# Kernel tuning notes

Hardware: AMD Instinct MI355X
Metric: run time of the kernel (lower is better)

## Reference

```python
import jax, jax.numpy as jnp
import numpy as np

NUM_HEADS = 4
HEAD_DIM = 64
BN_EPS = 1e-5

def _leaky_relu(x, slope=0.2):
    return jnp.where(x >= 0, x, slope * x)

def _gat_conv(x, W, a_src, a_dst, src, dst):
    # x: [N, F_in], W: [F_out, F_in], a_*: [H, D]; edges src/dst: [E]
    N = x.shape[0]
    h = (x @ W.T).reshape(N, NUM_HEADS, HEAD_DIM)          # [N, H, D]
    s_src = jnp.einsum('nhd,hd->nh', h, a_src)              # [N, H]
    s_dst = jnp.einsum('nhd,hd->nh', h, a_dst)              # [N, H]
    e = _leaky_relu(s_src[src] + s_dst[dst])                # [E, H]
    # segment softmax over edges grouped by dst; torch index_reduce_ starts
    # from zeros (include_self=True) -> max with 0
    e_max = jnp.maximum(jax.ops.segment_max(e, dst, num_segments=N), 0.0)
    e_exp = jnp.exp(e - e_max[dst])                         # [E, H]
    e_sum = jax.ops.segment_sum(e_exp, dst, num_segments=N) # [N, H]
    alpha = e_exp / jnp.maximum(e_sum[dst], 1e-9)           # [E, H]
    msg = h[src] * alpha[..., None]                         # [E, H, D]
    out = jax.ops.segment_sum(msg, dst, num_segments=N)     # [N, H, D]
    return out.reshape(N, NUM_HEADS * HEAD_DIM)

def _bn_eval(x, gamma, beta, mean, var):
    return (x - mean) * jax.lax.rsqrt(var + BN_EPS) * gamma + beta

def _elu(x):
    return jnp.where(x > 0, x, jnp.expm1(x))

def setup_inputs() -> dict:
    key = jax.random.key(0)
    ks = jax.random.split(key, 12)
    N, E, IN, HID, OUT = 50000, 500000, 256, 256, 64
    s = 0.05
    return {
        'x': jax.random.normal(ks[0], (N, IN), jnp.float32),
        'edge_index': jax.random.randint(ks[1], (2, E), 0, N, jnp.int64),
        'W1': jax.random.normal(ks[2], (HID, IN), jnp.float32) * s,
        'a_src1': jax.random.normal(ks[3], (NUM_HEADS, HEAD_DIM), jnp.float32) * s,
        'a_dst1': jax.random.normal(ks[4], (NUM_HEADS, HEAD_DIM), jnp.float32) * s,
        'bn1_gamma': jnp.ones((HID,), jnp.float32),
        'bn1_beta': jnp.zeros((HID,), jnp.float32),
        'bn1_mean': jnp.zeros((HID,), jnp.float32),
        'bn1_var': jnp.ones((HID,), jnp.float32),
        'W2': jax.random.normal(ks[5], (HID, HID), jnp.float32) * s,
        'a_src2': jax.random.normal(ks[6], (NUM_HEADS, HEAD_DIM), jnp.float32) * s,
        'a_dst2': jax.random.normal(ks[7], (NUM_HEADS, HEAD_DIM), jnp.float32) * s,
        'bn2_gamma': jnp.ones((HID,), jnp.float32),
        'bn2_beta': jnp.zeros((HID,), jnp.float32),
        'bn2_mean': jnp.zeros((HID,), jnp.float32),
        'bn2_var': jnp.ones((HID,), jnp.float32),
        'Wc': jax.random.normal(ks[8], (OUT, HID), jnp.float32) * s,
        'bc': jnp.zeros((OUT,), jnp.float32),
    }

def reference(x, edge_index, W1, a_src1, a_dst1, bn1_gamma, bn1_beta, bn1_mean, bn1_var,
              W2, a_src2, a_dst2, bn2_gamma, bn2_beta, bn2_mean, bn2_var, Wc, bc):
    src, dst = edge_index[0], edge_index[1]
    h = _gat_conv(x, W1, a_src1, a_dst1, src, dst)
    h = _elu(_bn_eval(h, bn1_gamma, bn1_beta, bn1_mean, bn1_var))
    h = _gat_conv(h, W2, a_src2, a_dst2, src, dst)
    h = _elu(_bn_eval(h, bn2_gamma, bn2_beta, bn2_mean, bn2_var))
    return h @ Wc.T + bc
```

## Files before the change

### kernel.cpp

```cpp
#include <hip/hip_runtime.h>

typedef __attribute__((ext_vector_type(8))) short short8;
typedef __attribute__((ext_vector_type(4))) float f32x4;

#define FF 256
#define NHEAD 4
#define HDIM 64
#define LDS_PITCH 264
#define BUCKET_CAP 64

__device__ __forceinline__ float bf2f(unsigned short u) {
  union { unsigned u; float f; } v; v.u = ((unsigned)u) << 16; return v.f;
}
__device__ __forceinline__ unsigned short f2bf(float f) {
  union { unsigned u; float f; } v; v.f = f;
  unsigned r = v.u + 0x7FFFu + ((v.u >> 16) & 1u);
  return (unsigned short)(r >> 16);
}

__device__ __forceinline__ short8 loadA8(const unsigned short* p) {
  return *(const short8*)p;
}
__device__ __forceinline__ short8 loadA8(const float* p) {
  f32x4 a = *(const f32x4*)p;
  f32x4 b = *(const f32x4*)(p + 4);
  short8 r;
  r[0] = (short)f2bf(a.x); r[1] = (short)f2bf(a.y);
  r[2] = (short)f2bf(a.z); r[3] = (short)f2bf(a.w);
  r[4] = (short)f2bf(b.x); r[5] = (short)f2bf(b.y);
  r[6] = (short)f2bf(b.z); r[7] = (short)f2bf(b.w);
  return r;
}

__global__ __launch_bounds__(256) void cvtw_kernel(
    const float* __restrict__ p0, int n0, const float* __restrict__ p1, int n1,
    const float* __restrict__ p2, int n2,
    unsigned short* __restrict__ o0, unsigned short* __restrict__ o1,
    unsigned short* __restrict__ o2, int* __restrict__ deg, int nz4) {
  int i = blockIdx.x * 256 + threadIdx.x;
  const float* in;
  unsigned short* out;
  int idx;
  if (i < n0) { in = p0; out = o0; idx = i; }
  else if (i < n0 + n1) { in = p1; out = o1; idx = i - n0; }
  else if (i < n0 + n1 + n2) { in = p2; out = o2; idx = i - n0 - n1; }
  else {
    int z = i - n0 - n1 - n2;
    if (z < nz4) ((int4*)deg)[z] = int4{0, 0, 0, 0};
    return;
  }
  f32x4 v = ((const f32x4*)in)[idx];
  ushort4 o;
  o.x = f2bf(v.x); o.y = f2bf(v.y); o.z = f2bf(v.z); o.w = f2bf(v.w);
  ((ushort4*)out)[idx] = o;
}

__global__ __launch_bounds__(256) void gemm1_scatter(
    const float* __restrict__ A, const unsigned short* __restrict__ B,
    unsigned short* __restrict__ Cb, const float* __restrict__ a_src,
    const float* __restrict__ a_dst, float* __restrict__ sS,
    float* __restrict__ sD, int M, int gemmBlocks,
    const int* __restrict__ src, const int* __restrict__ dst,
    int* __restrict__ deg, int* __restrict__ bucket, int E) {
  const int K = 256;
  int tid = threadIdx.x;

  if (blockIdx.x >= gemmBlocks) {
    int i = (blockIdx.x - gemmBlocks) * 256 + tid;
    if (i < E) {
      int d = dst[i];
      int s = src[i];
      if ((unsigned)d < (unsigned)M) {
        int p = atomicAdd(&deg[d], 1);
        if (p < BUCKET_CAP)
          bucket[(size_t)d * BUCKET_CAP + p] = ((unsigned)s < (unsigned)M) ? s : 0;
      }
    }
    return;
  }

  __shared__ unsigned short Atile[64 * LDS_PITCH];
  int wave = tid >> 6;
  int lane = tid & 63;
  int row0w = blockIdx.x * 64;
  int col0 = wave * 64;
  int lr = lane & 15;
  int quad = lane >> 4;

  short8 breg[4][8];
  {
    const unsigned short* Bp0 = B + (size_t)(col0 + lr) * K + quad * 8;
#pragma unroll
    for (int t = 0; t < 4; ++t)
#pragma unroll
      for (int kk = 0; kk < 8; ++kk)
        breg[t][kk] = *(const short8*)(Bp0 + (size_t)(16 * t) * K + kk * 32);
  }

  {
#pragma unroll
    for (int pass = 0; pass < 8; ++pass) {
      int c = tid + pass * 256;
      int row = c >> 5;
      int col8 = (c & 31) * 8;
      int grow = row0w + row;
      if (grow >= M) grow = M - 1;
      short8 v = loadA8(A + (size_t)grow * K + col8);
      *(short8*)(&Atile[row * LDS_PITCH + col8]) = v;
    }
  }
  __syncthreads();

  f32x4 acc[4][4];
#pragma unroll
  for (int rt = 0; rt < 4; ++rt)
#pragma unroll
    for (int t = 0; t < 4; ++t) acc[rt][t] = f32x4{0, 0, 0, 0};

#pragma unroll
  for (int kk = 0; kk < 8; ++kk) {
    short8 a[4];
#pragma unroll
    for (int rt = 0; rt < 4; ++rt)
      a[rt] = *(const short8*)(&Atile[(rt * 16 + lr) * LDS_PITCH + quad * 8 + kk * 32]);
#pragma unroll
    for (int rt = 0; rt < 4; ++rt)
#pragma unroll
      for (int t = 0; t < 4; ++t)
        acc[rt][t] = __builtin_amdgcn_mfma_f32_16x16x32_bf16(a[rt], breg[t][kk], acc[rt][t], 0, 0, 0);
  }

#pragma unroll
  for (int rt = 0; rt < 4; ++rt) {
#pragma unroll
    for (int t = 0; t < 4; ++t) {
#pragma unroll
      for (int r = 0; r < 4; ++r) {
        int row = row0w + rt * 16 + quad * 4 + r;
        if (row < M) {
          int col = col0 + 16 * t + lr;
          Cb[(size_t)row * FF + col] = f2bf(acc[rt][t][r]);
        }
      }
    }
  }

  {
    float asv[4], adv[4];
#pragma unroll
    for (int t = 0; t < 4; ++t) {
      asv[t] = a_src[col0 + 16 * t + lr];
      adv[t] = a_dst[col0 + 16 * t + lr];
    }
#pragma unroll
    for (int rt = 0; rt < 4; ++rt) {
#pragma unroll
      for (int r = 0; r < 4; ++r) {
        float ps = acc[rt][0][r] * asv[0] + acc[rt][1][r] * asv[1] +
                   acc[rt][2][r] * asv[2] + acc[rt][3][r] * asv[3];
        float pd = acc[rt][0][r] * adv[0] + acc[rt][1][r] * adv[1] +
                   acc[rt][2][r] * adv[2] + acc[rt][3][r] * adv[3];
#pragma unroll
        for (int sft = 1; sft < 16; sft <<= 1) {
          ps += __shfl_xor(ps, sft);
          pd += __shfl_xor(pd, sft);
        }
        if (lr == 0) {
          int row = row0w + rt * 16 + quad * 4 + r;
          if (row < M) {
            sS[row * NHEAD + wave] = ps;
            sD[row * NHEAD + wave] = pd;
          }
        }
      }
    }
  }
}

__global__ __launch_bounds__(256) void gemm_main(const unsigned short* __restrict__ A,
                                                 const unsigned short* __restrict__ B,
                                                 unsigned short* __restrict__ Cb,
                                                 const float* __restrict__ a_src,
                                                 const float* __restrict__ a_dst,
                                                 float* __restrict__ sS,
                                                 float* __restrict__ sD,
                                                 int M) {
  __shared__ unsigned short Atile[64 * LDS_PITCH];
  const int K = 256;
  int tid = threadIdx.x;
  int wave = tid >> 6;
  int lane = tid & 63;
  int row0w = blockIdx.x * 64;
  int col0 = wave * 64;
  int lr = lane & 15;
  int quad = lane >> 4;

  short8 breg[4][8];
  {
    const unsigned short* Bp0 = B + (size_t)(col0 + lr) * K + quad * 8;
#pragma unroll
    for (int t = 0; t < 4; ++t)
#pragma unroll
      for (int kk = 0; kk < 8; ++kk)
        breg[t][kk] = *(const short8*)(Bp0 + (size_t)(16 * t) * K + kk * 32);
  }

  {
#pragma unroll
    for (int pass = 0; pass < 8; ++pass) {
      int c = tid + pass * 256;
      int row = c >> 5;
      int col8 = (c & 31) * 8;
      int grow = row0w + row;
      if (grow >= M) grow = M - 1;
      short8 v = loadA8(A + (size_t)grow * K + col8);
      *(short8*)(&Atile[row * LDS_PITCH + col8]) = v;
    }
  }
  __syncthreads();

  f32x4 acc[4][4];
#pragma unroll
  for (int rt = 0; rt < 4; ++rt)
#pragma unroll
    for (int t = 0; t < 4; ++t) acc[rt][t] = f32x4{0, 0, 0, 0};

#pragma unroll
  for (int kk = 0; kk < 8; ++kk) {
    short8 a[4];
#pragma unroll
    for (int rt = 0; rt < 4; ++rt)
      a[rt] = *(const short8*)(&Atile[(rt * 16 + lr) * LDS_PITCH + quad * 8 + kk * 32]);
#pragma unroll
    for (int rt = 0; rt < 4; ++rt)
#pragma unroll
      for (int t = 0; t < 4; ++t)
        acc[rt][t] = __builtin_amdgcn_mfma_f32_16x16x32_bf16(a[rt], breg[t][kk], acc[rt][t], 0, 0, 0);
  }

#pragma unroll
  for (int rt = 0; rt < 4; ++rt) {
#pragma unroll
    for (int t = 0; t < 4; ++t) {
#pragma unroll
      for (int r = 0; r < 4; ++r) {
        int row = row0w + rt * 16 + quad * 4 + r;
        if (row < M) {
          int col = col0 + 16 * t + lr;
          Cb[(size_t)row * FF + col] = f2bf(acc[rt][t][r]);
        }
      }
    }
  }

  {
    float asv[4], adv[4];
#pragma unroll
    for (int t = 0; t < 4; ++t) {
      asv[t] = a_src[col0 + 16 * t + lr];
      adv[t] = a_dst[col0 + 16 * t + lr];
    }
#pragma unroll
    for (int rt = 0; rt < 4; ++rt) {
#pragma unroll
      for (int r = 0; r < 4; ++r) {
        float ps = acc[rt][0][r] * asv[0] + acc[rt][1][r] * asv[1] +
                   acc[rt][2][r] * asv[2] + acc[rt][3][r] * asv[3];
        float pd = acc[rt][0][r] * adv[0] + acc[rt][1][r] * adv[1] +
                   acc[rt][2][r] * adv[2] + acc[rt][3][r] * adv[3];
#pragma unroll
        for (int sft = 1; sft < 16; sft <<= 1) {
          ps += __shfl_xor(ps, sft);
          pd += __shfl_xor(pd, sft);
        }
        if (lr == 0) {
          int row = row0w + rt * 16 + quad * 4 + r;
          if (row < M) {
            sS[row * NHEAD + wave] = ps;
            sD[row * NHEAD + wave] = pd;
          }
        }
      }
    }
  }
}

__global__ __launch_bounds__(256) void gemm_head(const unsigned short* __restrict__ A,
                                                 const unsigned short* __restrict__ B,
                                                 float* __restrict__ Cf,
                                                 const float* __restrict__ bias,
                                                 int M) {
  const int K = 256;
  int wave = threadIdx.x >> 6;
  int lane = threadIdx.x & 63;
  int row0w = blockIdx.x * 64 + wave * 16;
  if (row0w >= M) return;
  int lr = lane & 15;
  int quad = lane >> 4;

  short8 breg[4][8];
  {
    const unsigned short* Bp0 = B + (size_t)lr * K + quad * 8;
#pragma unroll
    for (int t = 0; t < 4; ++t)
#pragma unroll
      for (int kk = 0; kk < 8; ++kk)
        breg[t][kk] = *(const short8*)(Bp0 + (size_t)(16 * t) * K + kk * 32);
  }

  const unsigned short* Ap;
  {
    int arow = row0w + lr;
    if (arow >= M) arow = M - 1;
    Ap = A + (size_t)arow * K + quad * 8;
  }

  f32x4 acc[4];
#pragma unroll
  for (int t = 0; t < 4; ++t) acc[t] = f32x4{0, 0, 0, 0};

#pragma unroll
  for (int kk = 0; kk < 8; ++kk) {
    short8 a = *(const short8*)(Ap + kk * 32);
#pragma unroll
    for (int t = 0; t < 4; ++t)
      acc[t] = __builtin_amdgcn_mfma_f32_16x16x32_bf16(a, breg[t][kk], acc[t], 0, 0, 0);
  }

#pragma unroll
  for (int t = 0; t < 4; ++t) {
#pragma unroll
    for (int r = 0; r < 4; ++r) {
      int row = row0w + quad * 4 + r;
      if (row < M) {
        int col = 16 * t + lr;
        Cf[(size_t)row * 64 + col] = acc[t][r] + bias[col];
      }
    }
  }
}

__global__ __launch_bounds__(256) void aggregate_kernel(
    const unsigned short* __restrict__ hprev, const float* __restrict__ sS,
    const float* __restrict__ sD, const int* __restrict__ deg,
    const int* __restrict__ bucket, const float* __restrict__ gamma,
    const float* __restrict__ beta, const float* __restrict__ mean,
    const float* __restrict__ var, unsigned short* __restrict__ hout, int N) {
  int wave = threadIdx.x >> 6;
  int lane = threadIdx.x & 63;
  int n = blockIdx.x * 4 + wave;
  if (n >= N) return;
  int hh = lane >> 4;
  int slot = lane & 15;
  int f0 = lane * 4;
  int srcBase = lane & 48;
  int dg = deg[n];
  if (dg > BUCKET_CAP) dg = BUCKET_CAP;
  int jb = n * BUCKET_CAP;
  int je = jb + dg;
  int jlast = je - 1;
  float sdv = sD[n * NHEAD + hh];
  float l = 0.f;
  float o0 = 0.f, o1 = 0.f, o2 = 0.f, o3 = 0.f;

  for (int c = jb; c < je; c += 16) {
    int j = c + slot;
    int jc = (j < jlast) ? j : jlast;
    int s = bucket[jc];
    float e = sS[s * NHEAD + hh] + sdv;
    e = (e >= 0.f) ? e : 0.2f * e;
    float w = (j < je) ? __expf(e) : 0.f;
    l += w;

    {
      uint2 u[8];
#pragma unroll
      for (int k = 0; k < 8; ++k) {
        int sk = __shfl(s, srcBase + k, 64);
        u[k] = *(const uint2*)(hprev + (size_t)sk * FF + f0);
      }
#pragma unroll
      for (int k = 0; k < 8; ++k) {
        float a = __shfl(w, srcBase + k, 64);
        o0 += a * __uint_as_float(u[k].x << 16);
        o1 += a * __uint_as_float(u[k].x & 0xffff0000u);
        o2 += a * __uint_as_float(u[k].y << 16);
        o3 += a * __uint_as_float(u[k].y & 0xffff0000u);
      }
    }
    if (c + 8 < je) {
      uint2 u[8];
#pragma unroll
      for (int k = 8; k < 16; ++k) {
        int sk = __shfl(s, srcBase + k, 64);
        u[k - 8] = *(const uint2*)(hprev + (size_t)sk * FF + f0);
      }
#pragma unroll
      for (int k = 8; k < 16; ++k) {
        float a = __shfl(w, srcBase + k, 64);
        o0 += a * __uint_as_float(u[k - 8].x << 16);
        o1 += a * __uint_as_float(u[k - 8].x & 0xffff0000u);
        o2 += a * __uint_as_float(u[k - 8].y << 16);
        o3 += a * __uint_as_float(u[k - 8].y & 0xffff0000u);
      }
    }
  }

  l += __shfl_xor(l, 1);
  l += __shfl_xor(l, 2);
  l += __shfl_xor(l, 4);
  l += __shfl_xor(l, 8);
  float li = 1.f / fmaxf(l, 1e-9f);

  f32x4 g = *(const f32x4*)(gamma + f0);
  f32x4 b = *(const f32x4*)(beta + f0);
  f32x4 mu = *(const f32x4*)(mean + f0);
  f32x4 vr = *(const f32x4*)(var + f0);
  float v0 = (o0 * li - mu.x) * rsqrtf(vr.x + 1e-5f) * g.x + b.x;
  float v1 = (o1 * li - mu.y) * rsqrtf(vr.y + 1e-5f) * g.y + b.y;
  float v2 = (o2 * li - mu.z) * rsqrtf(vr.z + 1e-5f) * g.z + b.z;
  float v3 = (o3 * li - mu.w) * rsqrtf(vr.w + 1e-5f) * g.w + b.w;
  v0 = (v0 > 0.f) ? v0 : expm1f(v0);
  v1 = (v1 > 0.f) ? v1 : expm1f(v1);
  v2 = (v2 > 0.f) ? v2 : expm1f(v2);
  v3 = (v3 > 0.f) ? v3 : expm1f(v3);
  ushort4 ov;
  ov.x = f2bf(v0); ov.y = f2bf(v1); ov.z = f2bf(v2); ov.w = f2bf(v3);
  *(ushort4*)(hout + (size_t)n * FF + f0) = ov;
}

extern "C" void kernel_launch(void* const* d_in, const int* in_sizes, int n_in,
                              void* d_out, int out_size, void* d_ws, size_t ws_size,
                              hipStream_t stream) {
  const float* x   = (const float*)d_in[0];
  const int* ei    = (const int*)d_in[1];
  const float* W1  = (const float*)d_in[2];
  const float* as1 = (const float*)d_in[3];
  const float* ad1 = (const float*)d_in[4];
  const float* g1  = (const float*)d_in[5];
  const float* b1  = (const float*)d_in[6];
  const float* m1  = (const float*)d_in[7];
  const float* v1  = (const float*)d_in[8];
  const float* W2  = (const float*)d_in[9];
  const float* as2 = (const float*)d_in[10];
  const float* ad2 = (const float*)d_in[11];
  const float* g2  = (const float*)d_in[12];
  const float* b2  = (const float*)d_in[13];
  const float* m2  = (const float*)d_in[14];
  const float* v2  = (const float*)d_in[15];
  const float* Wc  = (const float*)d_in[16];
  const float* bc  = (const float*)d_in[17];

  const int N = in_sizes[0] / FF;
  const int E = in_sizes[1] / 2;
  const int* srcIdx = ei;
  const int* dstIdx = ei + E;

  char* ws = (char*)d_ws;
  size_t off = 0;
  auto take = [&](size_t bytes) -> void* {
    void* p = ws + off;
    off += (bytes + 255) & ~(size_t)255;
    return p;
  };
  const int N4 = (N + 3) & ~3;
  int* deg        = (int*)take((size_t)N4 * 4);
  int* bucket     = (int*)take((size_t)N * BUCKET_CAP * 4);
  float* sS       = (float*)take((size_t)N * NHEAD * 4);
  float* sD       = (float*)take((size_t)N * NHEAD * 4);
  unsigned short* hpre = (unsigned short*)take((size_t)N * FF * 2);
  unsigned short* hact = (unsigned short*)take((size_t)N * FF * 2);
  unsigned short* w1b  = (unsigned short*)take((size_t)FF * FF * 2);
  unsigned short* w2b  = (unsigned short*)take((size_t)FF * FF * 2);
  unsigned short* wcb  = (unsigned short*)take((size_t)64 * FF * 2);

  const int tpb = 256;

  {
    int n0 = (FF * FF) / 4, n1 = (FF * FF) / 4, n2 = (64 * FF) / 4;
    int nz4 = N4 / 4;
    int tot = n0 + n1 + n2 + nz4;
    cvtw_kernel<<<(tot + tpb - 1) / tpb, tpb, 0, stream>>>(W1, n0, W2, n1, Wc, n2,
                                                           w1b, w2b, wcb, deg, nz4);
  }

  int aggBlocks = (N + 3) / 4;
  int gemmBlocks = (N + 63) / 64;
  int scatBlocks = (E + tpb - 1) / tpb;
  int headBlocks = (N + 63) / 64;

  gemm1_scatter<<<gemmBlocks + scatBlocks, 256, 0, stream>>>(
      x, w1b, hpre, as1, ad1, sS, sD, N, gemmBlocks, srcIdx, dstIdx, deg, bucket, E);
  aggregate_kernel<<<aggBlocks, 256, 0, stream>>>(hpre, sS, sD, deg, bucket,
                                                  g1, b1, m1, v1, hact, N);
  gemm_main<<<gemmBlocks, 256, 0, stream>>>(hact, w2b, hpre, as2, ad2, sS, sD, N);
  aggregate_kernel<<<aggBlocks, 256, 0, stream>>>(hpre, sS, sD, deg, bucket,
                                                  g2, b2, m2, v2, hact, N);
  gemm_head<<<headBlocks, 256, 0, stream>>>(hact, wcb, (float*)d_out, bc, N);
}
```

Measured before the change: 304.2 us.

## Fuse classifier head GEMM into second aggregation kernel epilogue

Removes the separate gemm_head launch by having the second aggregate kernel compute the 256->64 output projection per node in its epilogue. Wc is converted to a transposed packed-bf16 layout and staged in 32KB of LDS per block, and each wave's BN+ELU result row is written to LDS and dotted against Wc with scalar FMAs in fp32. This avoids writing the hidden activations to global memory and reading them back, but every 4-node block now reloads 32KB of weights into LDS, and the head runs on scalar FMAs instead of MFMA.

```diff
diff --git a/kernel.cpp b/kernel.cpp
--- a/kernel.cpp
+++ b/kernel.cpp
@@ -38,21 +38,30 @@
     unsigned short* __restrict__ o0, unsigned short* __restrict__ o1,
     unsigned short* __restrict__ o2, int* __restrict__ deg, int nz4) {
   int i = blockIdx.x * 256 + threadIdx.x;
-  const float* in;
-  unsigned short* out;
-  int idx;
-  if (i < n0) { in = p0; out = o0; idx = i; }
-  else if (i < n0 + n1) { in = p1; out = o1; idx = i - n0; }
-  else if (i < n0 + n1 + n2) { in = p2; out = o2; idx = i - n0 - n1; }
-  else {
+  if (i < n0 + n1) {
+    const float* in = (i < n0) ? p0 : p1;
+    unsigned short* out = (i < n0) ? o0 : o1;
+    int idx = (i < n0) ? i : i - n0;
+    f32x4 v = ((const f32x4*)in)[idx];
+    ushort4 o;
+    o.x = f2bf(v.x); o.y = f2bf(v.y); o.z = f2bf(v.z); o.w = f2bf(v.w);
+    ((ushort4*)out)[idx] = o;
+  } else if (i < n0 + n1 + n2) {
+    int idx = i - n0 - n1;
+    f32x4 v = ((const f32x4*)p2)[idx];
+    int e = idx * 4;
+    int c = e >> 8;
+    int f = e & 255;
+    unsigned u0 = (unsigned)f2bf(v.x) | ((unsigned)f2bf(v.y) << 16);
+    unsigned u1 = (unsigned)f2bf(v.z) | ((unsigned)f2bf(v.w) << 16);
+    unsigned* W32 = (unsigned*)o2;
+    int pb = f >> 1;
+    W32[(pb + 0) * 64 + c] = u0;
+    W32[(pb + 1) * 64 + c] = u1;
+  } else {
     int z = i - n0 - n1 - n2;
     if (z < nz4) ((int4*)deg)[z] = int4{0, 0, 0, 0};
-    return;
-  }
-  f32x4 v = ((const f32x4*)in)[idx];
-  ushort4 o;
-  o.x = f2bf(v.x); o.y = f2bf(v.y); o.z = f2bf(v.z); o.w = f2bf(v.w);
-  ((ushort4*)out)[idx] = o;
+  }
 }
 
 __global__ __launch_bounds__(256) void gemm1_scatter(
@@ -285,81 +294,44 @@
   }
 }
 
-__global__ __launch_bounds__(256) void gemm_head(const unsigned short* __restrict__ A,
-                                                 const unsigned short* __restrict__ B,
-                                                 float* __restrict__ Cf,
-                                                 const float* __restrict__ bias,
-                                                 int M) {
-  const int K = 256;
-  int wave = threadIdx.x >> 6;
-  int lane = threadIdx.x & 63;
-  int row0w = blockIdx.x * 64 + wave * 16;
-  if (row0w >= M) return;
-  int lr = lane & 15;
-  int quad = lane >> 4;
-
-  short8 breg[4][8];
-  {
-    const unsigned short* Bp0 = B + (size_t)lr * K + quad * 8;
-#pragma unroll
-    for (int t = 0; t < 4; ++t)
-#pragma unroll
-      for (int kk = 0; kk < 8; ++kk)
-        breg[t][kk] = *(const short8*)(Bp0 + (size_t)(16 * t) * K + kk * 32);
-  }
-
-  const unsigned short* Ap;
-  {
-    int arow = row0w + lr;
-    if (arow >= M) arow = M - 1;
-    Ap = A + (size_t)arow * K + quad * 8;
-  }
-
-  f32x4 acc[4];
-#pragma unroll
-  for (int t = 0; t < 4; ++t) acc[t] = f32x4{0, 0, 0, 0};
-
-#pragma unroll
-  for (int kk = 0; kk < 8; ++kk) {
-    short8 a = *(const short8*)(Ap + kk * 32);
-#pragma unroll
-    for (int t = 0; t < 4; ++t)
-      acc[t] = __builtin_amdgcn_mfma_f32_16x16x32_bf16(a, breg[t][kk], acc[t], 0, 0, 0);
-  }
-
-#pragma unroll
-  for (int t = 0; t < 4; ++t) {
-#pragma unroll
-    for (int r = 0; r < 4; ++r) {
-      int row = row0w + quad * 4 + r;
-      if (row < M) {
-        int col = 16 * t + lr;
-        Cf[(size_t)row * 64 + col] = acc[t][r] + bias[col];
-      }
-    }
-  }
-}
-
+template <bool WITH_HEAD>
 __global__ __launch_bounds__(256) void aggregate_kernel(
     const unsigned short* __restrict__ hprev, const float* __restrict__ sS,
     const float* __restrict__ sD, const int* __restrict__ deg,
     const int* __restrict__ bucket, const float* __restrict__ gamma,
     const float* __restrict__ beta, const float* __restrict__ mean,
-    const float* __restrict__ var, unsigned short* __restrict__ hout, int N) {
-  int wave = threadIdx.x >> 6;
-  int lane = threadIdx.x & 63;
+    const float* __restrict__ var, unsigned short* __restrict__ hout,
+    const unsigned short* __restrict__ wcT, const float* __restrict__ bc,
+    float* __restrict__ outF, int N) {
+  extern __shared__ char smem[];
+  unsigned* wcs = (unsigned*)smem;
+  float* hrow = (float*)(smem + 32768);
+
+  int tid = threadIdx.x;
+  int wave = tid >> 6;
+  int lane = tid & 63;
+
+  if constexpr (WITH_HEAD) {
+    const unsigned* wsrc = (const unsigned*)wcT;
+    for (int i = tid; i < 8192; i += 256) wcs[i] = wsrc[i];
+    __syncthreads();
+  }
+
   int n = blockIdx.x * 4 + wave;
-  if (n >= N) return;
+  bool active = (n < N);
+  if constexpr (!WITH_HEAD) {
+    if (!active) return;
+  }
   int hh = lane >> 4;
   int slot = lane & 15;
   int f0 = lane * 4;
   int srcBase = lane & 48;
-  int dg = deg[n];
+  int dg = active ? deg[n] : 0;
   if (dg > BUCKET_CAP) dg = BUCKET_CAP;
   int jb = n * BUCKET_CAP;
   int je = jb + dg;
   int jlast = je - 1;
-  float sdv = sD[n * NHEAD + hh];
+  float sdv = active ? sD[n * NHEAD + hh] : 0.f;
   float l = 0.f;
   float o0 = 0.f, o1 = 0.f, o2 = 0.f, o3 = 0.f;
 
@@ -424,9 +396,31 @@
   v1 = (v1 > 0.f) ? v1 : expm1f(v1);
   v2 = (v2 > 0.f) ? v2 : expm1f(v2);
   v3 = (v3 > 0.f) ? v3 : expm1f(v3);
-  ushort4 ov;
-  ov.x = f2bf(v0); ov.y = f2bf(v1); ov.z = f2bf(v2); ov.w = f2bf(v3);
-  *(ushort4*)(hout + (size_t)n * FF + f0) = ov;
+
+  if constexpr (!WITH_HEAD) {
+    ushort4 ov;
+    ov.x = f2bf(v0); ov.y = f2bf(v1); ov.z = f2bf(v2); ov.w = f2bf(v3);
+    *(ushort4*)(hout + (size_t)n * FF + f0) = ov;
+  } else {
+    if (active)
+      *(f32x4*)(&hrow[wave * 256 + f0]) = f32x4{v0, v1, v2, v3};
+    __syncthreads();
+    if (active) {
+      const float* hr = &hrow[wave * 256];
+      float acc = 0.f;
+#pragma unroll 8
+      for (int p4 = 0; p4 < 64; ++p4) {
+        f32x4 h = *(const f32x4*)(hr + p4 * 4);
+        unsigned wa = wcs[(2 * p4 + 0) * 64 + lane];
+        unsigned wb = wcs[(2 * p4 + 1) * 64 + lane];
+        acc += h.x * __uint_as_float(wa << 16);
+        acc += h.y * __uint_as_float(wa & 0xffff0000u);
+        acc += h.z * __uint_as_float(wb << 16);
+        acc += h.w * __uint_as_float(wb & 0xffff0000u);
+      }
+      outF[(size_t)n * 64 + lane] = acc + bc[lane];
+    }
+  }
 }
 
 extern "C" void kernel_launch(void* const* d_in, const int* in_sizes, int n_in,
@@ -487,14 +481,12 @@
   int aggBlocks = (N + 3) / 4;
   int gemmBlocks = (N + 63) / 64;
   int scatBlocks = (E + tpb - 1) / tpb;
-  int headBlocks = (N + 63) / 64;
 
   gemm1_scatter<<<gemmBlocks + scatBlocks, 256, 0, stream>>>(
       x, w1b, hpre, as1, ad1, sS, sD, N, gemmBlocks, srcIdx, dstIdx, deg, bucket, E);
-  aggregate_kernel<<<aggBlocks, 256, 0, stream>>>(hpre, sS, sD, deg, bucket,
-                                                  g1, b1, m1, v1, hact, N);
+  aggregate_kernel<false><<<aggBlocks, 256, 0, stream>>>(
+      hpre, sS, sD, deg, bucket, g1, b1, m1, v1, hact, wcb, bc, (float*)d_out, N);
   gemm_main<<<gemmBlocks, 256, 0, stream>>>(hact, w2b, hpre, as2, ad2, sS, sD, N);
-  aggregate_kernel<<<aggBlocks, 256, 0, stream>>>(hpre, sS, sD, deg, bucket,
-                                                  g2, b2, m2, v2, hact, N);
-  gemm_head<<<headBlocks, 256, 0, stream>>>(hact, wcb, (float*)d_out, bc, N);
-}
+  aggregate_kernel<true><<<aggBlocks, 256, 36864, stream>>>(
+      hpre, sS, sD, deg, bucket, g2, b2, m2, v2, hact, wcb, bc, (float*)d_out, N);
+}
```

Measured after the change: 342.0 us. +12.4%, slower.
